# Kernel optimization log

Hardware: AMD Instinct MI355X
Metric: run time of the kernel (lower is better)

The kernel has to match this reference:

```python
import jax, jax.numpy as jnp
import numpy as np
from jax import lax


def setup_inputs() -> dict:
    key = jax.random.key(0)
    x = jax.random.normal(key, (8, 1, 2048, 2048), dtype=jnp.float32)
    return {"x": x}


def reference(x):
    # torch.median over the whole tensor returns the LOWER median for even counts:
    # k-th smallest element with k = (n - 1) // 2.
    n = x.size
    med = jnp.sort(x.ravel())[(n - 1) // 2]

    # Threshold everything <= median to zero.
    thr = jnp.where(x > med, x, jnp.zeros_like(x))

    # 7x7 max pool, stride 1, padding 3 (torch pads with -inf), output same HxW.
    maxed = lax.reduce_window(
        thr,
        -jnp.inf,
        lax.max,
        window_dimensions=(1, 1, 7, 7),
        window_strides=(1, 1, 1, 1),
        padding=((0, 0), (0, 0), (3, 3), (3, 3)),
    )

    # Keep only local maxima (entries equal to their window max), scaled by score.
    out = jnp.where(thr == maxed, thr, jnp.zeros_like(thr))
    return out
```

## Files before the change

kernel.cpp:

```cpp
#include <hip/hip_runtime.h>
#include <math.h>

#define IMG_H 2048
#define IMG_W 2048
#define TX 64
#define TY 32
#define HALO 3
#define TILE_H (TY + 2 * HALO)
#define SIN_STR 76
#define SHM_STR 68
#define CAND_CAP (1u << 20)
#define CBUF 1024

__device__ __forceinline__ float4 fmax4(float4 a, float4 b) {
    return make_float4(fmaxf(a.x, b.x), fmaxf(a.y, b.y), fmaxf(a.z, b.z), fmaxf(a.w, b.w));
}

__device__ __forceinline__ unsigned f2key(unsigned u) {
    unsigned mask = (unsigned)(((int)u >> 31)) | 0x80000000u;
    return u ^ mask;
}
static inline unsigned f2key_host(float f) {
    union { float f; unsigned u; } c; c.f = f;
    unsigned mask = (unsigned)(((int)c.u >> 31)) | 0x80000000u;
    return c.u ^ mask;
}

__device__ __forceinline__ unsigned block_exscan(unsigned val, unsigned* tmp) {
    const int t = threadIdx.x;
    tmp[t] = val;
    __syncthreads();
#pragma unroll
    for (int off = 1; off < 256; off <<= 1) {
        unsigned v = (t >= off) ? tmp[t - off] : 0u;
        __syncthreads();
        tmp[t] += v;
        __syncthreads();
    }
    return tmp[t] - val;
}

template <int C>
__device__ __forceinline__ void find_crossing(const unsigned* bins, unsigned k,
                                              unsigned* tmp, unsigned* res) {
    unsigned s = 0;
#pragma unroll
    for (int j = 0; j < C; ++j) s += bins[threadIdx.x * C + j];
    unsigned ex = block_exscan(s, tmp);
    if (k >= ex && k < ex + s) {
        unsigned cum = ex;
        int b = threadIdx.x * C;
        while (cum + bins[b] <= k) { cum += bins[b]; ++b; }
        res[0] = (unsigned)b;
        res[1] = k - cum;
    }
    __syncthreads();
}

__global__ __launch_bounds__(256) void hist_window_kernel(
        const float4* __restrict__ x, int n4, unsigned* __restrict__ ghist,
        unsigned* __restrict__ ctrl, unsigned* __restrict__ candA,
        unsigned keyLo, unsigned keyHi) {
    __shared__ unsigned h[4 * 2048];
    __shared__ unsigned cbuf[CBUF];
    __shared__ unsigned ccnt, sbase, scnt;
    const int wave = threadIdx.x >> 6;
    unsigned* hw = &h[wave * 2048];
    for (int i = threadIdx.x; i < 4 * 2048; i += 256) h[i] = 0;
    if (threadIdx.x == 0) ccnt = 0;
    __syncthreads();
    const int stride = gridDim.x * blockDim.x;
    for (int i = blockIdx.x * blockDim.x + threadIdx.x; i < n4; i += stride) {
        float4 v = x[i];
        unsigned k0 = f2key(__float_as_uint(v.x));
        unsigned k1 = f2key(__float_as_uint(v.y));
        unsigned k2 = f2key(__float_as_uint(v.z));
        unsigned k3 = f2key(__float_as_uint(v.w));
        atomicAdd(&hw[k0 >> 21], 1u);
        atomicAdd(&hw[k1 >> 21], 1u);
        atomicAdd(&hw[k2 >> 21], 1u);
        atomicAdd(&hw[k3 >> 21], 1u);
        if (k0 > keyLo && k0 < keyHi) { unsigned p = atomicAdd(&ccnt, 1u); if (p < CBUF) cbuf[p] = k0; }
        if (k1 > keyLo && k1 < keyHi) { unsigned p = atomicAdd(&ccnt, 1u); if (p < CBUF) cbuf[p] = k1; }
        if (k2 > keyLo && k2 < keyHi) { unsigned p = atomicAdd(&ccnt, 1u); if (p < CBUF) cbuf[p] = k2; }
        if (k3 > keyLo && k3 < keyHi) { unsigned p = atomicAdd(&ccnt, 1u); if (p < CBUF) cbuf[p] = k3; }
    }
    __syncthreads();
    for (int b = threadIdx.x; b < 2048; b += 256) {
        unsigned s = h[b] + h[2048 + b] + h[4096 + b] + h[6144 + b];
        if (s) atomicAdd(&ghist[b], s);
    }
    if (threadIdx.x == 0) {
        unsigned c = ccnt;
        if (c > CBUF) { c = CBUF; atomicOr(&ctrl[3], 1u); }
        unsigned base = atomicAdd(&ctrl[2], c);
        if (base + c > CAND_CAP) {
            atomicOr(&ctrl[3], 1u);
            c = base < CAND_CAP ? CAND_CAP - base : 0;
        }
        sbase = base; scnt = c;
    }
    __syncthreads();
    for (unsigned i = threadIdx.x; i < scnt; i += 256) candA[sbase + i] = cbuf[i];
}

__global__ __launch_bounds__(256) void find_bucket_kernel(
        const unsigned* __restrict__ ghist, unsigned k, unsigned* __restrict__ ctrl,
        unsigned keyLo, unsigned keyHi) {
    __shared__ unsigned lh[2048];
    __shared__ unsigned tmp[256];
    __shared__ unsigned res[2];
    for (int i = threadIdx.x; i < 2048; i += 256) lh[i] = ghist[i];
    __syncthreads();
    find_crossing<8>(lh, k, tmp, res);
    if (threadIdx.x == 0) {
        unsigned b = res[0];
        ctrl[0] = b;
        ctrl[1] = res[1];
        unsigned lo = b << 21, hi = (b << 21) + 0x1FFFFFu;
        ctrl[4] = (lo > keyLo && hi < keyHi && ctrl[3] == 0u) ? 1u : 0u;
    }
}

__global__ __launch_bounds__(256) void compact_fallback_kernel(
        const float4* __restrict__ x, int n4, unsigned* __restrict__ ctrl,
        unsigned* __restrict__ candB) {
    if (ctrl[4]) return;
    const unsigned bucket = ctrl[0];
    const int stride = gridDim.x * blockDim.x;
    for (int i = blockIdx.x * blockDim.x + threadIdx.x; i < n4; i += stride) {
        float4 v = x[i];
        unsigned ks[4] = { f2key(__float_as_uint(v.x)), f2key(__float_as_uint(v.y)),
                           f2key(__float_as_uint(v.z)), f2key(__float_as_uint(v.w)) };
#pragma unroll
        for (int j = 0; j < 4; ++j)
            if ((ks[j] >> 21) == bucket) {
                unsigned p = atomicAdd(&ctrl[5], 1u);
                if (p < CAND_CAP) candB[p] = ks[j];
            }
    }
}

__global__ __launch_bounds__(256) void bucket_filter_kernel(
        const unsigned* __restrict__ ctrl_c, unsigned* __restrict__ ctrl,
        const unsigned* __restrict__ candA, unsigned* __restrict__ candC) {
    if (!ctrl_c[4]) return;
    const unsigned bucket = ctrl_c[0];
    unsigned M = ctrl_c[2];
    if (M > CAND_CAP) M = CAND_CAP;
    const int stride = gridDim.x * blockDim.x;
    for (unsigned i = blockIdx.x * blockDim.x + threadIdx.x; i < M; i += stride) {
        unsigned key = candA[i];
        if ((key >> 21) == bucket) {
            unsigned p = atomicAdd(&ctrl[6], 1u);
            if (p < CAND_CAP) candC[p] = key;
        }
    }
}

__global__ __launch_bounds__(256) void final_select_kernel(
        unsigned* __restrict__ ctrl, const unsigned* __restrict__ candC,
        const unsigned* __restrict__ candB, float* __restrict__ medp) {
    __shared__ unsigned h2[2048];
    __shared__ unsigned tmp[256];
    __shared__ unsigned res[2];
    const unsigned covered = ctrl[4];
    const unsigned* src = covered ? candC : candB;
    unsigned M = covered ? ctrl[6] : ctrl[5];
    if (M > CAND_CAP) M = CAND_CAP;
    const unsigned bucket = ctrl[0];
    const unsigned r = ctrl[1];

    for (int i = threadIdx.x; i < 2048; i += 256) h2[i] = 0;
    __syncthreads();
    for (unsigned i = threadIdx.x; i < M; i += 256) {
        unsigned key = src[i];
        if ((key >> 21) == bucket) atomicAdd(&h2[(key >> 10) & 0x7FFu], 1u);
    }
    __syncthreads();
    find_crossing<8>(h2, r, tmp, res);
    const unsigned pref = (bucket << 11) | res[0];
    const unsigned r2 = res[1];
    __syncthreads();

    for (int i = threadIdx.x; i < 1024; i += 256) h2[i] = 0;
    __syncthreads();
    for (unsigned i = threadIdx.x; i < M; i += 256) {
        unsigned key = src[i];
        if ((key >> 10) == pref) atomicAdd(&h2[key & 0x3FFu], 1u);
    }
    __syncthreads();
    find_crossing<4>(h2, r2, tmp, res);
    if (threadIdx.x == 0) {
        unsigned key = (pref << 10) | res[0];
        unsigned u = (key & 0x80000000u) ? (key ^ 0x80000000u) : ~key;
        *medp = __uint_as_float(u);
    }
}

__global__ __launch_bounds__(256, 6) void nms_kernel(const float* __restrict__ x,
                                                     float* __restrict__ out,
                                                     const float* __restrict__ medp) {
    __shared__ __align__(16) float sin_[TILE_H * SIN_STR];
    __shared__ __align__(16) float shm[TILE_H * SHM_STR];
    const float med = *medp;
    const int tx0 = blockIdx.x * TX;
    const int ty0 = blockIdx.y * TY;
    const size_t ib = (size_t)blockIdx.z * (size_t)(IMG_H * IMG_W);
    const float* img = x + ib;
    float* oimg = out + ib;
    const bool colsafe = (tx0 >= 4) && (tx0 + 68 <= IMG_W);

    for (int task = threadIdx.x; task < TILE_H * 18; task += 256) {
        int rr = task / 18;
        int c4 = task - rr * 18;
        int gy = ty0 + rr - HALO;
        int gx0 = tx0 - 4 + c4 * 4;
        float4 v;
        if ((unsigned)gy < (unsigned)IMG_H) {
            if (colsafe) {
                v = *(const float4*)(img + (size_t)gy * IMG_W + gx0);
                v.x = (v.x > med) ? v.x : 0.0f;
                v.y = (v.y > med) ? v.y : 0.0f;
                v.z = (v.z > med) ? v.z : 0.0f;
                v.w = (v.w > med) ? v.w : 0.0f;
            } else {
                float c[4];
#pragma unroll
                for (int j = 0; j < 4; ++j) {
                    int gx = gx0 + j;
                    if ((unsigned)gx < (unsigned)IMG_W) {
                        float xv = img[(size_t)gy * IMG_W + gx];
                        c[j] = (xv > med) ? xv : 0.0f;
                    } else c[j] = -INFINITY;
                }
                v = make_float4(c[0], c[1], c[2], c[3]);
            }
        } else {
            v = make_float4(-INFINITY, -INFINITY, -INFINITY, -INFINITY);
        }
        *(float4*)&sin_[rr * SIN_STR + c4 * 4] = v;
    }
    __syncthreads();

    for (int task = threadIdx.x; task < TILE_H * 4; task += 256) {
        int rr = task >> 2;
        int s = task & 3;
        int c0 = s * 16;
        const float* p = &sin_[rr * SIN_STR + c0];
        float v[24];
#pragma unroll
        for (int b = 0; b < 6; ++b) {
            float4 q = *(const float4*)(p + 4 * b);
            v[4 * b] = q.x; v[4 * b + 1] = q.y; v[4 * b + 2] = q.z; v[4 * b + 3] = q.w;
        }
        float m2[22];
#pragma unroll
        for (int j = 1; j <= 21; ++j) m2[j] = fmaxf(v[j], v[j + 1]);
        float m4[20];
#pragma unroll
        for (int j = 1; j <= 19; ++j) m4[j] = fmaxf(m2[j], m2[j + 2]);
        float o[16];
#pragma unroll
        for (int j = 0; j < 16; ++j) o[j] = fmaxf(m4[j + 1], m4[j + 4]);
        float* q = &shm[rr * SHM_STR + c0];
#pragma unroll
        for (int b = 0; b < 4; ++b)
            *(float4*)(q + 4 * b) = make_float4(o[4 * b], o[4 * b + 1], o[4 * b + 2], o[4 * b + 3]);
    }
    __syncthreads();

    {
        const int col4 = threadIdx.x & 15;
        const int r0 = (threadIdx.x >> 4) * 2;
        float4 v[8];
#pragma unroll
        for (int j = 0; j < 8; ++j) v[j] = *(const float4*)&shm[(r0 + j) * SHM_STR + col4 * 4];
        float4 m2[7];
#pragma unroll
        for (int j = 0; j < 7; ++j) m2[j] = fmax4(v[j], v[j + 1]);
        float4 m4[5];
#pragma unroll
        for (int j = 0; j < 5; ++j) m4[j] = fmax4(m2[j], m2[j + 2]);
        float4 ma = fmax4(m4[0], m4[3]);
        float4 mb = fmax4(m4[1], m4[4]);
        float4 ta = *(const float4*)&sin_[(r0 + HALO) * SIN_STR + col4 * 4 + 4];
        float4 tb = *(const float4*)&sin_[(r0 + 1 + HALO) * SIN_STR + col4 * 4 + 4];
        float4 oa = make_float4((ta.x == ma.x) ? ta.x : 0.0f, (ta.y == ma.y) ? ta.y : 0.0f,
                                (ta.z == ma.z) ? ta.z : 0.0f, (ta.w == ma.w) ? ta.w : 0.0f);
        float4 ob = make_float4((tb.x == mb.x) ? tb.x : 0.0f, (tb.y == mb.y) ? tb.y : 0.0f,
                                (tb.z == mb.z) ? tb.z : 0.0f, (tb.w == mb.w) ? tb.w : 0.0f);
        *(float4*)(oimg + (size_t)(ty0 + r0) * IMG_W + tx0 + col4 * 4) = oa;
        *(float4*)(oimg + (size_t)(ty0 + r0 + 1) * IMG_W + tx0 + col4 * 4) = ob;
    }
}

extern "C" void kernel_launch(void* const* d_in, const int* in_sizes, int n_in,
                              void* d_out, int out_size, void* d_ws, size_t ws_size,
                              hipStream_t stream) {
    const float* x = (const float*)d_in[0];
    float* out = (float*)d_out;
    const int n = in_sizes[0];
    const int n4 = n / 4;
    const unsigned k = (unsigned)((n - 1) / 2);

    unsigned char* ws = (unsigned char*)d_ws;
    unsigned* ghist = (unsigned*)ws;
    unsigned* ctrl = (unsigned*)(ws + 2048 * 4);
    float* medp = (float*)(ctrl + 7);
    unsigned* candA = (unsigned*)(ws + 2048 * 4 + 64);
    unsigned* candB = candA + CAND_CAP;
    unsigned* candC = candB + CAND_CAP;
    const size_t reserved = 2048 * 4 + 64;

    hipMemsetAsync(d_ws, 0, reserved, stream);

    const float W = 0.002f;
    const unsigned keyLo = f2key_host(-W);
    const unsigned keyHi = f2key_host(W);

    hist_window_kernel<<<1024, 256, 0, stream>>>((const float4*)x, n4, ghist, ctrl, candA, keyLo, keyHi);
    find_bucket_kernel<<<1, 256, 0, stream>>>(ghist, k, ctrl, keyLo, keyHi);
    compact_fallback_kernel<<<1024, 256, 0, stream>>>((const float4*)x, n4, ctrl, candB);
    bucket_filter_kernel<<<64, 256, 0, stream>>>(ctrl, ctrl, candA, candC);
    final_select_kernel<<<1, 256, 0, stream>>>(ctrl, candC, candB, medp);

    dim3 grid(IMG_W / TX, IMG_H / TY, n / (IMG_H * IMG_W));
    nms_kernel<<<grid, 256, 0, stream>>>(x, out, medp);
}
```

Before: 311.0 us.

## Replace histogram pass with below-window count and narrower candidate window for median

New measurement: 326.9 us. +5.1%, slower.

```diff
diff --git a/kernel.cpp b/kernel.cpp
--- a/kernel.cpp
+++ b/kernel.cpp
@@ -11,19 +11,27 @@
 #define SHM_STR 68
 #define CAND_CAP (1u << 20)
 #define CBUF 1024
+#define SEL_CAP 28672
 
 __device__ __forceinline__ float4 fmax4(float4 a, float4 b) {
     return make_float4(fmaxf(a.x, b.x), fmaxf(a.y, b.y), fmaxf(a.z, b.z), fmaxf(a.w, b.w));
+}
+
+typedef float __attribute__((ext_vector_type(4))) fvec4;
+__device__ __forceinline__ void nt_store4(float* p, float4 v) {
+    fvec4 w; w.x = v.x; w.y = v.y; w.z = v.z; w.w = v.w;
+    __builtin_nontemporal_store(w, (fvec4*)p);
 }
 
 __device__ __forceinline__ unsigned f2key(unsigned u) {
     unsigned mask = (unsigned)(((int)u >> 31)) | 0x80000000u;
     return u ^ mask;
 }
-static inline unsigned f2key_host(float f) {
-    union { float f; unsigned u; } c; c.f = f;
-    unsigned mask = (unsigned)(((int)c.u >> 31)) | 0x80000000u;
-    return c.u ^ mask;
+
+__device__ __forceinline__ bool is_covered(const unsigned* __restrict__ ctrl, unsigned k) {
+    unsigned cb = ctrl[7];
+    unsigned ca = ctrl[2]; if (ca > CAND_CAP) ca = CAND_CAP;
+    return (ctrl[3] == 0u) && (k >= cb) && (k - cb < ca);
 }
 
 __device__ __forceinline__ unsigned block_exscan(unsigned val, unsigned* tmp) {
@@ -57,39 +65,34 @@
     __syncthreads();
 }
 
-__global__ __launch_bounds__(256) void hist_window_kernel(
-        const float4* __restrict__ x, int n4, unsigned* __restrict__ ghist,
-        unsigned* __restrict__ ctrl, unsigned* __restrict__ candA,
-        unsigned keyLo, unsigned keyHi) {
-    __shared__ unsigned h[4 * 2048];
+__global__ __launch_bounds__(256) void pass1_kernel(
+        const float4* __restrict__ x, int n4, unsigned* __restrict__ ctrl,
+        unsigned* __restrict__ candA, float W) {
     __shared__ unsigned cbuf[CBUF];
+    __shared__ unsigned red[256];
     __shared__ unsigned ccnt, sbase, scnt;
-    const int wave = threadIdx.x >> 6;
-    unsigned* hw = &h[wave * 2048];
-    for (int i = threadIdx.x; i < 4 * 2048; i += 256) h[i] = 0;
     if (threadIdx.x == 0) ccnt = 0;
     __syncthreads();
+    const float lo = -W, hi = W;
+    unsigned cnt = 0;
     const int stride = gridDim.x * blockDim.x;
     for (int i = blockIdx.x * blockDim.x + threadIdx.x; i < n4; i += stride) {
         float4 v = x[i];
-        unsigned k0 = f2key(__float_as_uint(v.x));
-        unsigned k1 = f2key(__float_as_uint(v.y));
-        unsigned k2 = f2key(__float_as_uint(v.z));
-        unsigned k3 = f2key(__float_as_uint(v.w));
-        atomicAdd(&hw[k0 >> 21], 1u);
-        atomicAdd(&hw[k1 >> 21], 1u);
-        atomicAdd(&hw[k2 >> 21], 1u);
-        atomicAdd(&hw[k3 >> 21], 1u);
-        if (k0 > keyLo && k0 < keyHi) { unsigned p = atomicAdd(&ccnt, 1u); if (p < CBUF) cbuf[p] = k0; }
-        if (k1 > keyLo && k1 < keyHi) { unsigned p = atomicAdd(&ccnt, 1u); if (p < CBUF) cbuf[p] = k1; }
-        if (k2 > keyLo && k2 < keyHi) { unsigned p = atomicAdd(&ccnt, 1u); if (p < CBUF) cbuf[p] = k2; }
-        if (k3 > keyLo && k3 < keyHi) { unsigned p = atomicAdd(&ccnt, 1u); if (p < CBUF) cbuf[p] = k3; }
-    }
-    __syncthreads();
-    for (int b = threadIdx.x; b < 2048; b += 256) {
-        unsigned s = h[b] + h[2048 + b] + h[4096 + b] + h[6144 + b];
-        if (s) atomicAdd(&ghist[b], s);
-    }
+        cnt += (unsigned)(v.x <= lo) + (unsigned)(v.y <= lo) +
+               (unsigned)(v.z <= lo) + (unsigned)(v.w <= lo);
+        if (v.x > lo && v.x < hi) { unsigned p = atomicAdd(&ccnt, 1u); if (p < CBUF) cbuf[p] = f2key(__float_as_uint(v.x)); }
+        if (v.y > lo && v.y < hi) { unsigned p = atomicAdd(&ccnt, 1u); if (p < CBUF) cbuf[p] = f2key(__float_as_uint(v.y)); }
+        if (v.z > lo && v.z < hi) { unsigned p = atomicAdd(&ccnt, 1u); if (p < CBUF) cbuf[p] = f2key(__float_as_uint(v.z)); }
+        if (v.w > lo && v.w < hi) { unsigned p = atomicAdd(&ccnt, 1u); if (p < CBUF) cbuf[p] = f2key(__float_as_uint(v.w)); }
+    }
+    red[threadIdx.x] = cnt;
+    __syncthreads();
+#pragma unroll
+    for (int off = 128; off > 0; off >>= 1) {
+        if (threadIdx.x < off) red[threadIdx.x] += red[threadIdx.x + off];
+        __syncthreads();
+    }
+    if (threadIdx.x == 0) atomicAdd(&ctrl[7], red[0]);
     if (threadIdx.x == 0) {
         unsigned c = ccnt;
         if (c > CBUF) { c = CBUF; atomicOr(&ctrl[3], 1u); }
@@ -104,28 +107,46 @@
     for (unsigned i = threadIdx.x; i < scnt; i += 256) candA[sbase + i] = cbuf[i];
 }
 
+__global__ __launch_bounds__(256) void fallback_hist_kernel(
+        const float4* __restrict__ x, int n4, unsigned* __restrict__ ghist,
+        const unsigned* __restrict__ ctrl, unsigned k) {
+    if (is_covered(ctrl, k)) return;
+    __shared__ unsigned h[4 * 2048];
+    const int wave = threadIdx.x >> 6;
+    unsigned* hw = &h[wave * 2048];
+    for (int i = threadIdx.x; i < 4 * 2048; i += 256) h[i] = 0;
+    __syncthreads();
+    const int stride = gridDim.x * blockDim.x;
+    for (int i = blockIdx.x * blockDim.x + threadIdx.x; i < n4; i += stride) {
+        float4 v = x[i];
+        atomicAdd(&hw[f2key(__float_as_uint(v.x)) >> 21], 1u);
+        atomicAdd(&hw[f2key(__float_as_uint(v.y)) >> 21], 1u);
+        atomicAdd(&hw[f2key(__float_as_uint(v.z)) >> 21], 1u);
+        atomicAdd(&hw[f2key(__float_as_uint(v.w)) >> 21], 1u);
+    }
+    __syncthreads();
+    for (int b = threadIdx.x; b < 2048; b += 256) {
+        unsigned s = h[b] + h[2048 + b] + h[4096 + b] + h[6144 + b];
+        if (s) atomicAdd(&ghist[b], s);
+    }
+}
+
 __global__ __launch_bounds__(256) void find_bucket_kernel(
-        const unsigned* __restrict__ ghist, unsigned k, unsigned* __restrict__ ctrl,
-        unsigned keyLo, unsigned keyHi) {
+        const unsigned* __restrict__ ghist, unsigned k, unsigned* __restrict__ ctrl) {
+    if (is_covered(ctrl, k)) return;
     __shared__ unsigned lh[2048];
     __shared__ unsigned tmp[256];
     __shared__ unsigned res[2];
     for (int i = threadIdx.x; i < 2048; i += 256) lh[i] = ghist[i];
     __syncthreads();
     find_crossing<8>(lh, k, tmp, res);
-    if (threadIdx.x == 0) {
-        unsigned b = res[0];
-        ctrl[0] = b;
-        ctrl[1] = res[1];
-        unsigned lo = b << 21, hi = (b << 21) + 0x1FFFFFu;
-        ctrl[4] = (lo > keyLo && hi < keyHi && ctrl[3] == 0u) ? 1u : 0u;
-    }
+    if (threadIdx.x == 0) { ctrl[0] = res[0]; ctrl[1] = res[1]; }
 }
 
 __global__ __launch_bounds__(256) void compact_fallback_kernel(
         const float4* __restrict__ x, int n4, unsigned* __restrict__ ctrl,
-        unsigned* __restrict__ candB) {
-    if (ctrl[4]) return;
+        unsigned* __restrict__ candB, unsigned k) {
+    if (is_covered(ctrl, k)) return;
     const unsigned bucket = ctrl[0];
     const int stride = gridDim.x * blockDim.x;
     for (int i = blockIdx.x * blockDim.x + threadIdx.x; i < n4; i += stride) {
@@ -141,60 +162,90 @@
     }
 }
 
-__global__ __launch_bounds__(256) void bucket_filter_kernel(
-        const unsigned* __restrict__ ctrl_c, unsigned* __restrict__ ctrl,
-        const unsigned* __restrict__ candA, unsigned* __restrict__ candC) {
-    if (!ctrl_c[4]) return;
-    const unsigned bucket = ctrl_c[0];
-    unsigned M = ctrl_c[2];
-    if (M > CAND_CAP) M = CAND_CAP;
-    const int stride = gridDim.x * blockDim.x;
-    for (unsigned i = blockIdx.x * blockDim.x + threadIdx.x; i < M; i += stride) {
-        unsigned key = candA[i];
-        if ((key >> 21) == bucket) {
-            unsigned p = atomicAdd(&ctrl[6], 1u);
-            if (p < CAND_CAP) candC[p] = key;
-        }
-    }
-}
-
 __global__ __launch_bounds__(256) void final_select_kernel(
-        unsigned* __restrict__ ctrl, const unsigned* __restrict__ candC,
-        const unsigned* __restrict__ candB, float* __restrict__ medp) {
+        unsigned* __restrict__ ctrl, const unsigned* __restrict__ candA,
+        const unsigned* __restrict__ candB, float* __restrict__ medp, unsigned k) {
+    __shared__ unsigned keys[SEL_CAP];
     __shared__ unsigned h2[2048];
     __shared__ unsigned tmp[256];
     __shared__ unsigned res[2];
-    const unsigned covered = ctrl[4];
-    const unsigned* src = covered ? candC : candB;
-    unsigned M = covered ? ctrl[6] : ctrl[5];
-    if (M > CAND_CAP) M = CAND_CAP;
-    const unsigned bucket = ctrl[0];
-    const unsigned r = ctrl[1];
-
-    for (int i = threadIdx.x; i < 2048; i += 256) h2[i] = 0;
-    __syncthreads();
-    for (unsigned i = threadIdx.x; i < M; i += 256) {
-        unsigned key = src[i];
-        if ((key >> 21) == bucket) atomicAdd(&h2[(key >> 10) & 0x7FFu], 1u);
-    }
-    __syncthreads();
-    find_crossing<8>(h2, r, tmp, res);
-    const unsigned pref = (bucket << 11) | res[0];
-    const unsigned r2 = res[1];
-    __syncthreads();
-
-    for (int i = threadIdx.x; i < 1024; i += 256) h2[i] = 0;
-    __syncthreads();
-    for (unsigned i = threadIdx.x; i < M; i += 256) {
-        unsigned key = src[i];
-        if ((key >> 10) == pref) atomicAdd(&h2[key & 0x3FFu], 1u);
-    }
-    __syncthreads();
-    find_crossing<4>(h2, r2, tmp, res);
-    if (threadIdx.x == 0) {
-        unsigned key = (pref << 10) | res[0];
-        unsigned u = (key & 0x80000000u) ? (key ^ 0x80000000u) : ~key;
-        *medp = __uint_as_float(u);
+    const int t = threadIdx.x;
+    if (is_covered(ctrl, k)) {
+        unsigned M = ctrl[2];
+        const unsigned r = k - ctrl[7];
+        const bool staged = (M <= SEL_CAP);
+        if (staged) {
+            unsigned M4 = M >> 2;
+            const uint4* c4 = (const uint4*)candA;
+            for (unsigned i = t; i < M4; i += 256) {
+                uint4 q = c4[i];
+                keys[4 * i] = q.x; keys[4 * i + 1] = q.y;
+                keys[4 * i + 2] = q.z; keys[4 * i + 3] = q.w;
+            }
+            for (unsigned i = (M4 << 2) + t; i < M; i += 256) keys[i] = candA[i];
+        }
+        const unsigned* src = staged ? (const unsigned*)keys : candA;
+        __syncthreads();
+        for (unsigned i = t; i < 2048; i += 256) h2[i] = 0;
+        __syncthreads();
+        for (unsigned i = t; i < M; i += 256) atomicAdd(&h2[src[i] >> 21], 1u);
+        __syncthreads();
+        find_crossing<8>(h2, r, tmp, res);
+        const unsigned b1 = res[0];
+        const unsigned r1 = res[1];
+        __syncthreads();
+        for (unsigned i = t; i < 2048; i += 256) h2[i] = 0;
+        __syncthreads();
+        for (unsigned i = t; i < M; i += 256) {
+            unsigned key = src[i];
+            if ((key >> 21) == b1) atomicAdd(&h2[(key >> 10) & 0x7FFu], 1u);
+        }
+        __syncthreads();
+        find_crossing<8>(h2, r1, tmp, res);
+        const unsigned pref = (b1 << 11) | res[0];
+        const unsigned r2 = res[1];
+        __syncthreads();
+        for (unsigned i = t; i < 1024; i += 256) h2[i] = 0;
+        __syncthreads();
+        for (unsigned i = t; i < M; i += 256) {
+            unsigned key = src[i];
+            if ((key >> 10) == pref) atomicAdd(&h2[key & 0x3FFu], 1u);
+        }
+        __syncthreads();
+        find_crossing<4>(h2, r2, tmp, res);
+        if (t == 0) {
+            unsigned key = (pref << 10) | res[0];
+            unsigned u = (key & 0x80000000u) ? (key ^ 0x80000000u) : ~key;
+            *medp = __uint_as_float(u);
+        }
+    } else {
+        unsigned M = ctrl[5]; if (M > CAND_CAP) M = CAND_CAP;
+        const unsigned bucket = ctrl[0];
+        const unsigned r = ctrl[1];
+        for (int i = t; i < 2048; i += 256) h2[i] = 0;
+        __syncthreads();
+        for (unsigned i = t; i < M; i += 256) {
+            unsigned key = candB[i];
+            if ((key >> 21) == bucket) atomicAdd(&h2[(key >> 10) & 0x7FFu], 1u);
+        }
+        __syncthreads();
+        find_crossing<8>(h2, r, tmp, res);
+        const unsigned pref = (bucket << 11) | res[0];
+        const unsigned r2 = res[1];
+        __syncthreads();
+        for (int i = t; i < 1024; i += 256) h2[i] = 0;
+        __syncthreads();
+        for (unsigned i = t; i < M; i += 256) {
+            unsigned key = candB[i];
+            if ((key >> 10) == pref) atomicAdd(&h2[key & 0x3FFu], 1u);
+        }
+        __syncthreads();
+        find_crossing<4>(h2, r2, tmp, res);
+        if (t == 0) {
+            unsigned key = (pref << 10) | res[0];
+            unsigned u = (key & 0x80000000u) ? (key ^ 0x80000000u) : ~key;
+            *medp = __uint_as_float(u);
+        }
     }
 }
 
@@ -290,8 +341,8 @@
                                 (ta.z == ma.z) ? ta.z : 0.0f, (ta.w == ma.w) ? ta.w : 0.0f);
         float4 ob = make_float4((tb.x == mb.x) ? tb.x : 0.0f, (tb.y == mb.y) ? tb.y : 0.0f,
                                 (tb.z == mb.z) ? tb.z : 0.0f, (tb.w == mb.w) ? tb.w : 0.0f);
-        *(float4*)(oimg + (size_t)(ty0 + r0) * IMG_W + tx0 + col4 * 4) = oa;
-        *(float4*)(oimg + (size_t)(ty0 + r0 + 1) * IMG_W + tx0 + col4 * 4) = ob;
+        nt_store4(oimg + (size_t)(ty0 + r0) * IMG_W + tx0 + col4 * 4, oa);
+        nt_store4(oimg + (size_t)(ty0 + r0 + 1) * IMG_W + tx0 + col4 * 4, ob);
     }
 }
 
@@ -307,23 +358,20 @@
     unsigned char* ws = (unsigned char*)d_ws;
     unsigned* ghist = (unsigned*)ws;
     unsigned* ctrl = (unsigned*)(ws + 2048 * 4);
-    float* medp = (float*)(ctrl + 7);
+    float* medp = (float*)(ctrl + 8);
     unsigned* candA = (unsigned*)(ws + 2048 * 4 + 64);
     unsigned* candB = candA + CAND_CAP;
-    unsigned* candC = candB + CAND_CAP;
     const size_t reserved = 2048 * 4 + 64;
 
     hipMemsetAsync(d_ws, 0, reserved, stream);
 
-    const float W = 0.002f;
-    const unsigned keyLo = f2key_host(-W);
-    const unsigned keyHi = f2key_host(W);
-
-    hist_window_kernel<<<1024, 256, 0, stream>>>((const float4*)x, n4, ghist, ctrl, candA, keyLo, keyHi);
-    find_bucket_kernel<<<1, 256, 0, stream>>>(ghist, k, ctrl, keyLo, keyHi);
-    compact_fallback_kernel<<<1024, 256, 0, stream>>>((const float4*)x, n4, ctrl, candB);
-    bucket_filter_kernel<<<64, 256, 0, stream>>>(ctrl, ctrl, candA, candC);
-    final_select_kernel<<<1, 256, 0, stream>>>(ctrl, candC, candB, medp);
+    const float W = 0.001f;
+
+    pass1_kernel<<<1024, 256, 0, stream>>>((const float4*)x, n4, ctrl, candA, W);
+    fallback_hist_kernel<<<1024, 256, 0, stream>>>((const float4*)x, n4, ghist, ctrl, k);
+    find_bucket_kernel<<<1, 256, 0, stream>>>(ghist, k, ctrl);
+    compact_fallback_kernel<<<1024, 256, 0, stream>>>((const float4*)x, n4, ctrl, candB, k);
+    final_select_kernel<<<1, 256, 0, stream>>>(ctrl, candA, candB, medp, k);
 
     dim3 grid(IMG_W / TX, IMG_H / TY, n / (IMG_H * IMG_W));
     nms_kernel<<<grid, 256, 0, stream>>>(x, out, medp);
```
